# Kernel optimization log

Hardware: AMD Instinct MI355X
Metric: run time of the kernel (lower is better)

Reference implementation:

```python
import jax, jax.numpy as jnp
import numpy as np

H_BINS = 64
SIGMA = 0.02
EPS = 1e-6


def setup_inputs() -> dict:
    key = jax.random.key(0)
    x = jax.random.uniform(key, (8, 3, 256, 256), dtype=jnp.float32)
    return {"x": x}


def reference(x):
    h = H_BINS
    L = x.shape[0]
    x = jnp.clip(x, 0.0, 1.0)
    I = x.reshape(L, 3, -1)                      # [L,3,N]
    Iy = jnp.sqrt(jnp.sum(I * I, axis=1) + EPS)  # [L,N] pixel intensity
    logs = jnp.log(I + EPS)                      # [L,3,N]
    # per-channel log-chromaticity: for c=0:(u=l0-l1, v=l0-l2); c=1:(l1-l0, l1-l2); c=2:(l2-l0, l2-l1)
    cu = jnp.array([1, 0, 0])
    cv = jnp.array([2, 2, 1])
    U = logs - logs[:, cu, :]                    # [L,3,N]
    V = logs - logs[:, cv, :]                    # [L,3,N]
    offset = jnp.linspace(-3.0, 3.0, h, dtype=jnp.float32)  # [h]
    inv_s2 = jnp.float32(1.0 / (SIGMA * SIGMA))
    # RBF-like (inverse-quadratic) soft binning kernels: [L,3,N,h]
    Ku = 1.0 / (1.0 + jnp.square(U[..., None] - offset) * inv_s2)
    Kv = 1.0 / (1.0 + jnp.square(V[..., None] - offset) * inv_s2)
    # weighted outer-product reduction over pixels -> [L,3,h,h]
    hists = jnp.einsum('ln,lcnu,lcnv->lcuv', Iy, Ku, Kv)
    # normalize each sample by its total mass
    total = jnp.sum(hists, axis=(1, 2, 3), keepdims=True)
    return hists / (total + EPS)
```

## Files before the change

### kernel.cpp

```cpp
#include <hip/hip_runtime.h>

#define H 64
#define NPIX 65536
#define LBATCH 8
#define LC 24
#define S_CHUNKS 32
#define PB 2048
#define EPSF 1e-6f
#define LN2_50 34.6573590f

typedef _Float16 h8 __attribute__((ext_vector_type(8)));
typedef __fp16   g2 __attribute__((ext_vector_type(2)));
typedef float f32x16 __attribute__((ext_vector_type(16)));
union H8u { h8 v8; g2 v2[4]; };

#define KEV(d) __builtin_amdgcn_rcpf(fmaf((d), (d), 1.0f))
#define PK(a, b) __builtin_amdgcn_cvt_pkrtz((a), (b))

__global__ __launch_bounds__(256) void hist_zero(float* __restrict__ out) {
    out[blockIdx.x * 256 + threadIdx.x] = 0.0f;
}

__global__ __launch_bounds__(256, 3) void hist_main(const float* __restrict__ x,
                                                    float* __restrict__ out) {
    __shared__ float sU[PB];
    __shared__ float sV[PB];
    __shared__ float sW[PB];
    __shared__ float sHist[H * H];

    const int tid  = threadIdx.x;
    const int wv   = tid >> 6;
    const int lane = tid & 63;
    const int hf   = lane >> 5;
    const int ln   = lane & 31;
    const int lc   = blockIdx.y;
    const int l    = lc / 3;
    const int c    = lc - 3 * l;

    #pragma unroll
    for (int r = 0; r < 4; r++)
        *(float4*)&sHist[(r * 256 + tid) * 4] = make_float4(0.f, 0.f, 0.f, 0.f);

    const float* __restrict__ x0p = x + (l * 3 + 0) * NPIX;
    const float* __restrict__ x1p = x + (l * 3 + 1) * NPIX;
    const float* __restrict__ x2p = x + (l * 3 + 2) * NPIX;
    const int base = blockIdx.x * PB;

    #pragma unroll
    for (int pass = 0; pass < 2; pass++) {
        const int ploc = pass * 1024 + tid * 4;
        const float4 r0 = *(const float4*)&x0p[base + ploc];
        const float4 r1 = *(const float4*)&x1p[base + ploc];
        const float4 r2 = *(const float4*)&x2p[base + ploc];
        float4 U4, V4, W4;
        #define PREP(E) { \
            const float v0 = fminf(fmaxf(r0.E, 0.0f), 1.0f); \
            const float v1 = fminf(fmaxf(r1.E, 0.0f), 1.0f); \
            const float v2 = fminf(fmaxf(r2.E, 0.0f), 1.0f); \
            W4.E = __builtin_amdgcn_sqrtf(fmaf(v0, v0, fmaf(v1, v1, fmaf(v2, v2, EPSF)))); \
            const float lg0 = __builtin_amdgcn_logf(v0 + EPSF); \
            const float lg1 = __builtin_amdgcn_logf(v1 + EPSF); \
            const float lg2 = __builtin_amdgcn_logf(v2 + EPSF); \
            float U, V; \
            if (c == 0)      { U = lg0 - lg1; V = lg0 - lg2; } \
            else if (c == 1) { U = lg1 - lg0; V = lg1 - lg2; } \
            else             { U = lg2 - lg0; V = lg2 - lg1; } \
            U4.E = LN2_50 * U; V4.E = LN2_50 * V; }
        PREP(x) PREP(y) PREP(z) PREP(w)
        #undef PREP
        *(float4*)&sU[ploc] = U4;
        *(float4*)&sV[ploc] = V4;
        *(float4*)&sW[ploc] = W4;
    }
    __syncthreads();

    const float step50 = 50.0f * (6.0f / 63.0f);
    const float ou0 = -150.0f + step50 * (float)ln;
    const float ou1 = ou0 + step50 * 32.0f;

    f32x16 acc00, acc01, acc10, acc11;
    #pragma unroll
    for (int i = 0; i < 16; i++) { acc00[i] = 0.f; acc01[i] = 0.f; acc10[i] = 0.f; acc11[i] = 0.f; }

    const int wbase = wv * 512;
    #pragma unroll 2
    for (int ks = 0; ks < 32; ks++) {
        const int kb = wbase + ks * 16 + hf * 8;
        const float4 ua = *(const float4*)&sU[kb];
        const float4 ub = *(const float4*)&sU[kb + 4];
        const float4 va = *(const float4*)&sV[kb];
        const float4 vb = *(const float4*)&sV[kb + 4];
        const float4 wa = *(const float4*)&sW[kb];
        const float4 wb = *(const float4*)&sW[kb + 4];
        H8u A0, A1, B0, B1;
        A0.v2[0] = PK(wa.x * KEV(ua.x - ou0), wa.y * KEV(ua.y - ou0));
        A0.v2[1] = PK(wa.z * KEV(ua.z - ou0), wa.w * KEV(ua.w - ou0));
        A0.v2[2] = PK(wb.x * KEV(ub.x - ou0), wb.y * KEV(ub.y - ou0));
        A0.v2[3] = PK(wb.z * KEV(ub.z - ou0), wb.w * KEV(ub.w - ou0));
        A1.v2[0] = PK(wa.x * KEV(ua.x - ou1), wa.y * KEV(ua.y - ou1));
        A1.v2[1] = PK(wa.z * KEV(ua.z - ou1), wa.w * KEV(ua.w - ou1));
        A1.v2[2] = PK(wb.x * KEV(ub.x - ou1), wb.y * KEV(ub.y - ou1));
        A1.v2[3] = PK(wb.z * KEV(ub.z - ou1), wb.w * KEV(ub.w - ou1));
        B0.v2[0] = PK(KEV(va.x - ou0), KEV(va.y - ou0));
        B0.v2[1] = PK(KEV(va.z - ou0), KEV(va.w - ou0));
        B0.v2[2] = PK(KEV(vb.x - ou0), KEV(vb.y - ou0));
        B0.v2[3] = PK(KEV(vb.z - ou0), KEV(vb.w - ou0));
        B1.v2[0] = PK(KEV(va.x - ou1), KEV(va.y - ou1));
        B1.v2[1] = PK(KEV(va.z - ou1), KEV(va.w - ou1));
        B1.v2[2] = PK(KEV(vb.x - ou1), KEV(vb.y - ou1));
        B1.v2[3] = PK(KEV(vb.z - ou1), KEV(vb.w - ou1));
        acc00 = __builtin_amdgcn_mfma_f32_32x32x16_f16(A0.v8, B0.v8, acc00, 0, 0, 0);
        acc01 = __builtin_amdgcn_mfma_f32_32x32x16_f16(A0.v8, B1.v8, acc01, 0, 0, 0);
        acc10 = __builtin_amdgcn_mfma_f32_32x32x16_f16(A1.v8, B0.v8, acc10, 0, 0, 0);
        acc11 = __builtin_amdgcn_mfma_f32_32x32x16_f16(A1.v8, B1.v8, acc11, 0, 0, 0);
    }

    #pragma unroll
    for (int r = 0; r < 16; r++) {
        const int row = (r & 3) + 8 * (r >> 2) + 4 * hf;
        atomicAdd(&sHist[row * 64 + ln],             acc00[r]);
        atomicAdd(&sHist[row * 64 + 32 + ln],        acc01[r]);
        atomicAdd(&sHist[(row + 32) * 64 + ln],      acc10[r]);
        atomicAdd(&sHist[(row + 32) * 64 + 32 + ln], acc11[r]);
    }
    __syncthreads();

    float* __restrict__ g = out + lc * (H * H);
    #pragma unroll
    for (int r = 0; r < 16; r++) {
        const int i = r * 256 + tid;
        unsafeAtomicAdd(&g[i], sHist[i]);
    }
}

__global__ __launch_bounds__(256) void hist_finish(float* __restrict__ out) {
    const int l = blockIdx.x;
    float* __restrict__ p = out + l * 3 * H * H;
    float s = 0.0f;
    #pragma unroll
    for (int it = 0; it < 12; it++) {
        const float4 v = *(const float4*)&p[(it * 256 + threadIdx.x) * 4];
        s += (v.x + v.y) + (v.z + v.w);
    }
    #pragma unroll
    for (int off = 32; off > 0; off >>= 1) s += __shfl_down(s, off, 64);
    __shared__ float ps[4];
    if ((threadIdx.x & 63) == 0) ps[threadIdx.x >> 6] = s;
    __syncthreads();
    const float T = (ps[0] + ps[1]) + (ps[2] + ps[3]);
    const float inv = 1.0f / (T + EPSF);
    #pragma unroll
    for (int it = 0; it < 12; it++) {
        float4 v = *(const float4*)&p[(it * 256 + threadIdx.x) * 4];
        v.x *= inv; v.y *= inv; v.z *= inv; v.w *= inv;
        *(float4*)&p[(it * 256 + threadIdx.x) * 4] = v;
    }
}

extern "C" void kernel_launch(void* const* d_in, const int* in_sizes, int n_in,
                              void* d_out, int out_size, void* d_ws, size_t ws_size,
                              hipStream_t stream) {
    const float* x = (const float*)d_in[0];
    float* out = (float*)d_out;

    hipLaunchKernelGGL(hist_zero,   dim3(LC * H * H / 256), dim3(256), 0, stream, out);
    hipLaunchKernelGGL(hist_main,   dim3(S_CHUNKS, LC),     dim3(256), 0, stream, x, out);
    hipLaunchKernelGGL(hist_finish, dim3(LBATCH),           dim3(256), 0, stream, out);
}
```

Before: 150.7 us.

## Compute soft-bin kernels in packed fp16 with Newton reciprocal and fp16 LDS staging

Replaces the per-element fp32 rcp kernel evaluation with packed half2 arithmetic. The reciprocal starts from a bit-trick seed and is refined by two Newton steps, with the argument clamped to keep it in fp16 range. U, V and W are staged in LDS as fp16, and pixel chunks are halved while the block count doubles, with launch bounds raised to target 4 blocks per CU. The aim is to cut the VALU and transcendental cost that feeds the MFMAs, at the cost of fp16 rounding of the scaled log-chromaticity values and twice as many global atomic flushes of the histogram.

After: 207.3 us. 1.38x slower.

```diff
diff --git a/kernel.cpp b/kernel.cpp
--- a/kernel.cpp
+++ b/kernel.cpp
@@ -4,28 +4,43 @@
 #define NPIX 65536
 #define LBATCH 8
 #define LC 24
-#define S_CHUNKS 32
-#define PB 2048
+#define S_CHUNKS 64
+#define PB 1024
 #define EPSF 1e-6f
 #define LN2_50 34.6573590f
 
 typedef _Float16 h8 __attribute__((ext_vector_type(8)));
-typedef __fp16   g2 __attribute__((ext_vector_type(2)));
+typedef _Float16 h4 __attribute__((ext_vector_type(4)));
+typedef _Float16 h2 __attribute__((ext_vector_type(2)));
+typedef short    s2 __attribute__((ext_vector_type(2)));
 typedef float f32x16 __attribute__((ext_vector_type(16)));
-union H8u { h8 v8; g2 v2[4]; };
+union H8p { h8 v8; h2 h[4]; };
 
-#define KEV(d) __builtin_amdgcn_rcpf(fmaf((d), (d), 1.0f))
-#define PK(a, b) __builtin_amdgcn_cvt_pkrtz((a), (b))
+#if __has_builtin(__builtin_elementwise_fma)
+#define FMA2(a, b, c) __builtin_elementwise_fma((a), (b), (c))
+#else
+#define FMA2(a, b, c) ((a) * (b) + (c))
+#endif
+
+static __device__ __forceinline__ h2 kev2(h2 u2, h2 o2, h2 one2, h2 two2,
+                                          h2 clamp2, s2 magic2) {
+    const h2 d  = u2 - o2;
+    const h2 xx = __builtin_elementwise_min(FMA2(d, d, one2), clamp2);
+    h2 y = __builtin_bit_cast(h2, (s2)(magic2 - __builtin_bit_cast(s2, xx)));
+    y = y * FMA2(-xx, y, two2);
+    y = y * FMA2(-xx, y, two2);
+    return y;
+}
 
 __global__ __launch_bounds__(256) void hist_zero(float* __restrict__ out) {
     out[blockIdx.x * 256 + threadIdx.x] = 0.0f;
 }
 
-__global__ __launch_bounds__(256, 3) void hist_main(const float* __restrict__ x,
+__global__ __launch_bounds__(256, 4) void hist_main(const float* __restrict__ x,
                                                     float* __restrict__ out) {
-    __shared__ float sU[PB];
-    __shared__ float sV[PB];
-    __shared__ float sW[PB];
+    __shared__ _Float16 sUh[PB];
+    __shared__ _Float16 sVh[PB];
+    __shared__ _Float16 sWh[PB];
     __shared__ float sHist[H * H];
 
     const int tid  = threadIdx.x;
@@ -46,9 +61,8 @@
     const float* __restrict__ x2p = x + (l * 3 + 2) * NPIX;
     const int base = blockIdx.x * PB;
 
-    #pragma unroll
-    for (int pass = 0; pass < 2; pass++) {
-        const int ploc = pass * 1024 + tid * 4;
+    {
+        const int ploc = tid * 4;
         const float4 r0 = *(const float4*)&x0p[base + ploc];
         const float4 r1 = *(const float4*)&x1p[base + ploc];
         const float4 r2 = *(const float4*)&x2p[base + ploc];
@@ -68,47 +82,43 @@
             U4.E = LN2_50 * U; V4.E = LN2_50 * V; }
         PREP(x) PREP(y) PREP(z) PREP(w)
         #undef PREP
-        *(float4*)&sU[ploc] = U4;
-        *(float4*)&sV[ploc] = V4;
-        *(float4*)&sW[ploc] = W4;
+        *(h4*)&sUh[ploc] = h4{(_Float16)U4.x, (_Float16)U4.y, (_Float16)U4.z, (_Float16)U4.w};
+        *(h4*)&sVh[ploc] = h4{(_Float16)V4.x, (_Float16)V4.y, (_Float16)V4.z, (_Float16)V4.w};
+        *(h4*)&sWh[ploc] = h4{(_Float16)W4.x, (_Float16)W4.y, (_Float16)W4.z, (_Float16)W4.w};
     }
     __syncthreads();
 
     const float step50 = 50.0f * (6.0f / 63.0f);
     const float ou0 = -150.0f + step50 * (float)ln;
     const float ou1 = ou0 + step50 * 32.0f;
+    const _Float16 oh0 = (_Float16)ou0;
+    const _Float16 oh1 = (_Float16)ou1;
+    const h2 o0_2 = {oh0, oh0};
+    const h2 o1_2 = {oh1, oh1};
+    const h2 one2   = {(_Float16)1.0f, (_Float16)1.0f};
+    const h2 two2   = {(_Float16)2.0f, (_Float16)2.0f};
+    const h2 clamp2 = {(_Float16)16384.0f, (_Float16)16384.0f};
+    const s2 magic2 = {(short)0x779A, (short)0x779A};
 
     f32x16 acc00, acc01, acc10, acc11;
     #pragma unroll
     for (int i = 0; i < 16; i++) { acc00[i] = 0.f; acc01[i] = 0.f; acc10[i] = 0.f; acc11[i] = 0.f; }
 
-    const int wbase = wv * 512;
+    const int wbase = wv * 256;
     #pragma unroll 2
-    for (int ks = 0; ks < 32; ks++) {
+    for (int ks = 0; ks < 16; ks++) {
         const int kb = wbase + ks * 16 + hf * 8;
-        const float4 ua = *(const float4*)&sU[kb];
-        const float4 ub = *(const float4*)&sU[kb + 4];
-        const float4 va = *(const float4*)&sV[kb];
-        const float4 vb = *(const float4*)&sV[kb + 4];
-        const float4 wa = *(const float4*)&sW[kb];
-        const float4 wb = *(const float4*)&sW[kb + 4];
-        H8u A0, A1, B0, B1;
-        A0.v2[0] = PK(wa.x * KEV(ua.x - ou0), wa.y * KEV(ua.y - ou0));
-        A0.v2[1] = PK(wa.z * KEV(ua.z - ou0), wa.w * KEV(ua.w - ou0));
-        A0.v2[2] = PK(wb.x * KEV(ub.x - ou0), wb.y * KEV(ub.y - ou0));
-        A0.v2[3] = PK(wb.z * KEV(ub.z - ou0), wb.w * KEV(ub.w - ou0));
-        A1.v2[0] = PK(wa.x * KEV(ua.x - ou1), wa.y * KEV(ua.y - ou1));
-        A1.v2[1] = PK(wa.z * KEV(ua.z - ou1), wa.w * KEV(ua.w - ou1));
-        A1.v2[2] = PK(wb.x * KEV(ub.x - ou1), wb.y * KEV(ub.y - ou1));
-        A1.v2[3] = PK(wb.z * KEV(ub.z - ou1), wb.w * KEV(ub.w - ou1));
-        B0.v2[0] = PK(KEV(va.x - ou0), KEV(va.y - ou0));
-        B0.v2[1] = PK(KEV(va.z - ou0), KEV(va.w - ou0));
-        B0.v2[2] = PK(KEV(vb.x - ou0), KEV(vb.y - ou0));
-        B0.v2[3] = PK(KEV(vb.z - ou0), KEV(vb.w - ou0));
-        B1.v2[0] = PK(KEV(va.x - ou1), KEV(va.y - ou1));
-        B1.v2[1] = PK(KEV(va.z - ou1), KEV(va.w - ou1));
-        B1.v2[2] = PK(KEV(vb.x - ou1), KEV(vb.y - ou1));
-        B1.v2[3] = PK(KEV(vb.z - ou1), KEV(vb.w - ou1));
+        H8p U, V, W, A0, A1, B0, B1;
+        U.v8 = *(const h8*)&sUh[kb];
+        V.v8 = *(const h8*)&sVh[kb];
+        W.v8 = *(const h8*)&sWh[kb];
+        #pragma unroll
+        for (int q = 0; q < 4; q++) {
+            A0.h[q] = W.h[q] * kev2(U.h[q], o0_2, one2, two2, clamp2, magic2);
+            A1.h[q] = W.h[q] * kev2(U.h[q], o1_2, one2, two2, clamp2, magic2);
+            B0.h[q] = kev2(V.h[q], o0_2, one2, two2, clamp2, magic2);
+            B1.h[q] = kev2(V.h[q], o1_2, one2, two2, clamp2, magic2);
+        }
         acc00 = __builtin_amdgcn_mfma_f32_32x32x16_f16(A0.v8, B0.v8, acc00, 0, 0, 0);
         acc01 = __builtin_amdgcn_mfma_f32_32x32x16_f16(A0.v8, B1.v8, acc01, 0, 0, 0);
         acc10 = __builtin_amdgcn_mfma_f32_32x32x16_f16(A1.v8, B0.v8, acc10, 0, 0, 0);
```
